# Kernel tuning notes

Measured on AMD Instinct MI355X. Metric: run time of the kernel, lower is better.

Reference implementation:

```python
import jax, jax.numpy as jnp
import numpy as np
from jax import lax

NUM_CLASSES = 5
CONF_THRESH = 0.6
NMS_THRESH = 0.2
NUM_TOPK = 64          # min(topk=1000, 64) as in post_process
STRIDES = (8, 16, 32)
FMP = ((160, 160), (80, 80), (40, 40))  # 1280x1280 input
BATCH = 128


def setup_inputs() -> dict:
    key = jax.random.key(0)
    ks = jax.random.split(key, 9)
    d = {}
    i = 0
    for name, (h, w) in zip(("8", "16", "32"), FMP):
        hw = h * w
        d["obj" + name] = jax.random.normal(ks[i], (BATCH, hw, 1), jnp.float32); i += 1
        d["cls" + name] = jax.random.normal(ks[i], (BATCH, hw, NUM_CLASSES), jnp.float32); i += 1
        d["reg" + name] = jax.random.normal(ks[i], (BATCH, hw, 4), jnp.float32); i += 1
    return d


def make_anchors(h, w, stride):
    ay, ax = jnp.meshgrid(jnp.arange(h), jnp.arange(w), indexing="ij")
    xy = jnp.stack([ax, ay], axis=-1).astype(jnp.float32).reshape(-1, 2)
    return (xy + 0.5) * stride  # [HW, 2]


def decode_boxes(reg, anchors, stride):
    # ctr = reg[:, :2]*stride + anchor;  wh = exp(reg[:, 2:])*stride
    ctr = reg[:, :2] * stride + anchors
    wh = jnp.exp(reg[:, 2:]) * stride
    return jnp.concatenate([ctr - 0.5 * wh, ctr + 0.5 * wh], axis=-1)  # x1y1x2y2


def iou_matrix(b):
    # Faithful to YOLO.nms: areas un-clamped, intersection w/h clamped at 1e-10
    x1, y1, x2, y2 = b[:, 0], b[:, 1], b[:, 2], b[:, 3]
    areas = (x2 - x1) * (y2 - y1)
    xx1 = jnp.maximum(x1[:, None], x1[None, :])
    yy1 = jnp.maximum(y1[:, None], y1[None, :])
    xx2 = jnp.minimum(x2[:, None], x2[None, :])
    yy2 = jnp.minimum(y2[:, None], y2[None, :])
    w = jnp.maximum(1e-10, xx2 - xx1)
    h = jnp.maximum(1e-10, yy2 - yy1)
    inter = w * h
    return inter / (areas[:, None] + areas[None, :] - inter)


def nms_keep(iou, valid):
    # Greedy NMS on score-sorted candidates: fixed-length sequential suppression.
    n = iou.shape[0]
    idx = jnp.arange(n)
    def body(i, keep):
        sup = keep[i] & (iou[i] > NMS_THRESH) & (idx > i)
        return keep & jnp.logical_not(sup)
    return lax.fori_loop(0, n, body, valid)


def _single_image(obj8, cls8, reg8, obj16, cls16, reg16, obj32, cls32, reg32):
    levels = ((obj8, cls8, reg8), (obj16, cls16, reg16), (obj32, cls32, reg32))
    sc, lb, bx, vd = [], [], [], []
    for lvl, (obj, cls, reg) in enumerate(levels):
        h, w = FMP[lvl]
        s = STRIDES[lvl]
        anchors = make_anchors(h, w, s)
        boxes = decode_boxes(reg, anchors, s)                      # [HW, 4]
        scores = jnp.sqrt(jax.nn.sigmoid(obj) * jax.nn.sigmoid(cls)).reshape(-1)  # [HW*C]
        top_s, top_i = lax.top_k(scores, NUM_TOPK)
        a_idx = top_i // NUM_CLASSES
        labels = top_i % NUM_CLASSES
        sc.append(top_s)
        lb.append(labels)
        bx.append(boxes[a_idx])
        vd.append(top_s > CONF_THRESH)
    scores = jnp.concatenate(sc)          # [192]
    labels = jnp.concatenate(lb)
    boxes = jnp.concatenate(bx)           # [192, 4]
    valid = jnp.concatenate(vd)
    # Global score order (within each class this matches the per-class argsort)
    order = jnp.argsort(-scores)
    scores, labels, boxes, valid = scores[order], labels[order], boxes[order], valid[order]
    # Class-offset trick: boxes of different classes have IoU ~ 0 -> exactly per-class NMS
    off = labels.astype(jnp.float32) * (2.0 * jnp.max(jnp.abs(boxes)) + 1.0)
    keep = nms_keep(iou_matrix(boxes + off[:, None]), valid)
    scores = jnp.where(keep, scores, 0.0)
    boxes = jnp.where(keep[:, None], boxes, 0.0)
    labels = jnp.where(keep, labels, -1)
    return boxes, scores, labels


def reference(obj8, cls8, reg8, obj16, cls16, reg16, obj32, cls32, reg32):
    # Batched (vmapped) version of inference_single_image's decode+postprocess.
    # Returns fixed-size masked outputs: boxes [B,192,4], scores [B,192], labels [B,192].
    return jax.vmap(_single_image)(obj8, cls8, reg8, obj16, cls16, reg16, obj32, cls32, reg32)
```

## Files before the change

kernel.cpp:

```cpp
#include <hip/hip_runtime.h>


#define NUM_CLASSES 5
#define CONF_THRESH 0.6f
#define NMS_THRESH  0.2f
#define TOPK   64
#define BATCH  128
#define TOTK   192
#define NCH    21
#define CHUNK  1600
#define SCAP   1024
#define NTHR   320
#define WCAP   1024

typedef unsigned long long u64;
typedef unsigned int u32;
typedef unsigned short u16;


__device__ inline u32 wave_sort64_desc_u32(u32 v, int lane) {
  #pragma unroll
  for (int k = 2; k <= 64; k <<= 1) {
    #pragma unroll
    for (int j = k >> 1; j > 0; j >>= 1) {
      u32 o = __shfl_xor(v, j, 64);
      bool keepMax = (((lane & k) == 0) != ((lane & j) != 0));
      v = keepMax ? (v > o ? v : o) : (v < o ? v : o);
    }
  }
  return v;
}

__device__ inline u64 wave_sort64_desc(u64 v, int lane) {
  #pragma unroll
  for (int k = 2; k <= 64; k <<= 1) {
    #pragma unroll
    for (int j = k >> 1; j > 0; j >>= 1) {
      u64 o = __shfl_xor(v, j, 64);
      bool keepMax = (((lane & k) == 0) != ((lane & j) != 0));
      v = keepMax ? (v > o ? v : o) : (v < o ? v : o);
    }
  }
  return v;
}

__device__ __forceinline__ u64 u64max(u64 a, u64 b) { return a > b ? a : b; }
__device__ __forceinline__ u64 u64min(u64 a, u64 b) { return a < b ? a : b; }

__device__ __forceinline__ u64 bmerge64_desc(u64 v, int lane) {
  #pragma unroll
  for (int j = 32; j > 0; j >>= 1) {
    u64 o = __shfl_xor(v, j, 64);
    v = ((lane & j) == 0) ? u64max(v, o) : u64min(v, o);
  }
  return v;
}

__device__ __forceinline__ u64 merge_top64(u64 a, u64 brev, int lane) {
  return bmerge64_desc(u64max(a, brev), lane);
}

__device__ __forceinline__ u64 merge4_top64(u64 a, u64 brev, u64 c, u64 drev, int lane) {
  u64 ab = merge_top64(a, brev, lane);
  u64 cd = merge_top64(c, drev, lane);
  u64 cdr = __shfl(cd, 63 - lane, 64);
  return merge_top64(ab, cdr, lane);
}

__device__ inline u64 score_key(float so, float cv, int idx) {
  float sc = 1.0f / (1.0f + expf(-cv));
  float s  = sqrtf(__fmul_rn(so, sc));
  return ((u64)__float_as_uint(s) << 32) | (u32)(~(u32)idx);
}

__device__ inline float sigmoidf(float x) { return 1.0f / (1.0f + expf(-x)); }

__global__ __launch_bounds__(NTHR) void scan_kernel(
    const float* __restrict__ obj8,  const float* __restrict__ cls8,
    const float* __restrict__ obj16, const float* __restrict__ cls16,
    const float* __restrict__ obj32, const float* __restrict__ cls32,
    u64* __restrict__ ws_part) {
  __shared__ u64 keys[SCAP];
  __shared__ u16 wl[WCAP];
  __shared__ int cnt;
  __shared__ int wcnt;
  __shared__ u32 sthr[5];

  const int bx  = blockIdx.x;
  const int img = bx / NCH;
  const int c   = bx - img * NCH;
  const int t   = threadIdx.x;
  const int lane = t & 63, wv = t >> 6;

  const float *obj, *cls;
  int hw, off;
  if (c < 16)      { obj = obj8;  cls = cls8;  hw = 25600; off = c * CHUNK; }
  else if (c < 20) { obj = obj16; cls = cls16; hw = 6400;  off = (c - 16) * CHUNK; }
  else             { obj = obj32; cls = cls32; hw = 1600;  off = 0; }
  obj += (size_t)img * hw + off;
  cls += ((size_t)img * hw + off) * NUM_CLASSES;

  float ff[25];
  {
    const float4* c4 = (const float4*)cls + (size_t)t * 5;
    float4 q0 = c4[0], q1 = c4[1], q2 = c4[2], q3 = c4[3], q4 = c4[4];
    float4 ov = ((const float4*)obj)[t];
    float cv[20] = { q0.x,q0.y,q0.z,q0.w, q1.x,q1.y,q1.z,q1.w,
                     q2.x,q2.y,q2.z,q2.w, q3.x,q3.y,q3.z,q3.w,
                     q4.x,q4.y,q4.z,q4.w };
    float dob[4] = { 1.0f + __expf(-ov.x), 1.0f + __expf(-ov.y),
                     1.0f + __expf(-ov.z), 1.0f + __expf(-ov.w) };
    #pragma unroll
    for (int a = 0; a < 4; ++a)
      #pragma unroll
      for (int j = 0; j < 5; ++j)
        ff[a * 5 + j] = dob[a] * (1.0f + __expf(-cv[a * 5 + j]));
    float ot = obj[1280 + t];
    float dot_ = 1.0f + __expf(-ot);
    #pragma unroll
    for (int j = 0; j < 5; ++j) {
      float cvt = cls[(1280 + t) * 5 + j];
      ff[20 + j] = dot_ * (1.0f + __expf(-cvt));
    }
  }

  float pmin = ff[0];
  #pragma unroll
  for (int i = 1; i < 25; ++i) pmin = fminf(pmin, ff[i]);
  u32 srt = wave_sort64_desc_u32(__float_as_uint(pmin), lane);
  if (lane == 48) sthr[wv] = srt;
  if (t == 0) { cnt = 0; wcnt = 0; }
  __syncthreads();
  u64 thr; float thr_inv;
  {
    float pmax = __uint_as_float(sthr[0]);
    pmax = fmaxf(pmax, __uint_as_float(sthr[1]));
    pmax = fmaxf(pmax, __uint_as_float(sthr[2]));
    pmax = fmaxf(pmax, __uint_as_float(sthr[3]));
    pmax = fmaxf(pmax, __uint_as_float(sthr[4]));
    float ts = sqrtf(__fdiv_rn(1.0f, pmax)) * (1.0f - 1e-4f);
    thr = ((u64)__float_as_uint(ts) << 32) - 1ull;
    thr_inv = __fdiv_rn(1.0f, __fmul_rn(__fmul_rn(ts, ts), 1.0f - 2e-4f));
  }

  #pragma unroll
  for (int a = 0; a < 4; ++a)
    #pragma unroll
    for (int j = 0; j < 5; ++j)
      if (ff[a * 5 + j] <= thr_inv) {
        int p = atomicAdd(&wcnt, 1);
        if (p < WCAP) wl[p] = (u16)(((4 * t + a) << 3) | j);
      }
  #pragma unroll
  for (int j = 0; j < 5; ++j)
    if (ff[20 + j] <= thr_inv) {
      int p = atomicAdd(&wcnt, 1);
      if (p < WCAP) wl[p] = (u16)(((1280 + t) << 3) | j);
    }
  __syncthreads();
  const int wc = wcnt;

  if (wc <= WCAP) {
    for (int i = t; i < wc; i += NTHR) {
      u32 cd = (u32)wl[i];
      int al = (int)(cd >> 3);
      int jj = (int)(cd & 7u);
      float o   = obj[al];
      float cvv = cls[al * 5 + jj];
      u64 key = score_key(sigmoidf(o), cvv, (off + al) * NUM_CLASSES + jj);
      if (key > thr) { int p = atomicAdd(&cnt, 1); if (p < SCAP) keys[p] = key; }
    }
  } else {
    #pragma unroll
    for (int a = 0; a < 4; ++a)
      #pragma unroll
      for (int j = 0; j < 5; ++j)
        if (ff[a * 5 + j] <= thr_inv) {
          int al = 4 * t + a;
          u64 key = score_key(sigmoidf(obj[al]), cls[al * 5 + j],
                              (off + al) * NUM_CLASSES + j);
          if (key > thr) { int p = atomicAdd(&cnt, 1); if (p < SCAP) keys[p] = key; }
        }
    #pragma unroll
    for (int j = 0; j < 5; ++j)
      if (ff[20 + j] <= thr_inv) {
        int al = 1280 + t;
        u64 key = score_key(sigmoidf(obj[al]), cls[al * 5 + j],
                            (off + al) * NUM_CLASSES + j);
        if (key > thr) { int p = atomicAdd(&cnt, 1); if (p < SCAP) keys[p] = key; }
      }
  }
  __syncthreads();
  int cs = cnt; if (cs > SCAP) cs = SCAP;
  __syncthreads();

  if (cs > 512) {
    int m = 64; while (m < cs) m <<= 1;
    for (int i = cs + t; i < m; i += NTHR) keys[i] = 0ull;
    for (int kk = 2; kk <= m; kk <<= 1) {
      for (int j = kk >> 1; j > 0; j >>= 1) {
        __syncthreads();
        for (int i = t; i < m; i += NTHR) {
          int ixj = i ^ j;
          if (ixj > i) {
            u64 a = keys[i], b = keys[ixj];
            bool sw = ((i & kk) == 0) ? (a < b) : (a > b);
            if (sw) { keys[i] = b; keys[ixj] = a; }
          }
        }
      }
    }
    __syncthreads();
  } else {
    int npow = 1; while (npow * 64 < cs) npow <<= 1;
    for (int i = cs + t; i < npow * 64; i += NTHR) keys[i] = 0ull;
    __syncthreads();
    for (int r = wv; r < npow; r += 5) {
      u64 v = wave_sort64_desc(keys[r * 64 + lane], lane);
      keys[r * 64 + lane] = v;
    }
    __syncthreads();
    for (int half = npow >> 1; half >= 1; half >>= 1) {
      u64 res = 0ull;
      if (wv < half) {
        u64 a    = keys[(2 * wv) * 64 + lane];
        u64 brev = keys[(2 * wv + 1) * 64 + 63 - lane];
        res = merge_top64(a, brev, lane);
      }
      __syncthreads();
      if (wv < half) keys[wv * 64 + lane] = res;
      __syncthreads();
    }
  }
  if (t < TOPK) ws_part[(size_t)bx * TOPK + t] = keys[t];
}

__global__ __launch_bounds__(256) void merge_nms_kernel(
    const u64* __restrict__ ws_part,
    const float* __restrict__ reg8, const float* __restrict__ reg16, const float* __restrict__ reg32,
    float* __restrict__ out) {
  __shared__ u64   lds_runs[256];
  __shared__ u64   lvlkeys[TOTK];
  __shared__ u64   skeys[TOTK];
  __shared__ int   slb[TOTK];
  __shared__ float sbx[TOTK * 4];
  __shared__ float sX1[TOTK], sY1[TOTK], sX2[TOTK], sY2[TOTK], sA[TOTK];
  __shared__ u64   rows[TOTK * 3];
  __shared__ u64   svalid[3];
  __shared__ u64   skeep[3];
  __shared__ float lmarr[3];

  const int img  = blockIdx.x;
  const int t    = threadIdx.x;
  const int lane = t & 63, wv = t >> 6;

  const u64* pbase = ws_part + (size_t)img * NCH * TOPK;

  {
    const u64* q = pbase + (size_t)(4 * wv) * TOPK;
    u64 a    = q[lane];
    u64 brev = q[64 + 63 - lane];
    u64 c    = q[128 + lane];
    u64 drev = q[192 + 63 - lane];
    lds_runs[wv * 64 + lane] = merge4_top64(a, brev, c, drev, lane);
    if (wv == 3) lvlkeys[128 + lane] = pbase[20 * TOPK + lane];
  }
  __syncthreads();

  if (wv == 0) {
    u64 a    = lds_runs[lane];
    u64 brev = lds_runs[64 + 63 - lane];
    u64 c    = lds_runs[128 + lane];
    u64 drev = lds_runs[192 + 63 - lane];
    lvlkeys[lane] = merge4_top64(a, brev, c, drev, lane);
  } else if (wv == 1) {
    const u64* q = pbase + (size_t)16 * TOPK;
    u64 a    = q[lane];
    u64 brev = q[64 + 63 - lane];
    u64 c    = q[128 + lane];
    u64 drev = q[192 + 63 - lane];
    lvlkeys[64 + lane] = merge4_top64(a, brev, c, drev, lane);
  }
  __syncthreads();

  if (wv == 0) {
    const u64 HIMASK = 0xFFFFFFFF00000000ull;
    u64 s0 = (lvlkeys[lane] & HIMASK) | (u32)(~(u32)lane);
    int i1 = 64 + 63 - lane;
    u64 s1r = (lvlkeys[i1] & HIMASK) | (u32)(~(u32)i1);
    int i2 = 128 + 63 - lane;
    u64 s2r = (lvlkeys[i2] & HIMASK) | (u32)(~(u32)i2);
    u64 hi_ = bmerge64_desc(u64max(s0, s1r), lane);
    u64 lo_ = bmerge64_desc(u64min(s0, s1r), lane);
    u64 R1   = u64max(lo_, s2r);
    u64 out0 = bmerge64_desc(u64max(hi_, R1), lane);
    u64 out1 = bmerge64_desc(u64min(hi_, R1), lane);
    u64 out2 = bmerge64_desc(u64min(lo_, s2r), lane);
    skeys[lane]       = out0;
    skeys[64 + lane]  = out1;
    skeys[128 + lane] = out2;
  } else {
    int idx = t - 64;
    const float* reg; int w; int hw; float stride;
    if (wv == 1)      { reg = reg8;  w = 160; hw = 25600; stride = 8.0f;  }
    else if (wv == 2) { reg = reg16; w = 80;  hw = 6400;  stride = 16.0f; }
    else              { reg = reg32; w = 40;  hw = 1600;  stride = 32.0f; }
    reg += (size_t)img * hw * 4;
    u64 key = lvlkeys[idx];
    u32 raw = ~((u32)key);
    int a = (int)(raw / NUM_CLASSES);
    int c = (int)(raw - (u32)a * NUM_CLASSES);
    int ix = a % w, iy = a / w;
    float ax = __fmul_rn((float)ix + 0.5f, stride);
    float ay = __fmul_rn((float)iy + 0.5f, stride);
    float r0 = reg[a*4+0], r1 = reg[a*4+1], r2 = reg[a*4+2], r3 = reg[a*4+3];
    float cx = __fadd_rn(__fmul_rn(r0, stride), ax);
    float cy = __fadd_rn(__fmul_rn(r1, stride), ay);
    float wd = __fmul_rn(expf(r2), stride);
    float ht = __fmul_rn(expf(r3), stride);
    float x1 = __fsub_rn(cx, __fmul_rn(0.5f, wd));
    float y1 = __fsub_rn(cy, __fmul_rn(0.5f, ht));
    float x2 = __fadd_rn(cx, __fmul_rn(0.5f, wd));
    float y2 = __fadd_rn(cy, __fmul_rn(0.5f, ht));
    slb[idx] = c;
    sbx[idx*4+0] = x1; sbx[idx*4+1] = y1;
    sbx[idx*4+2] = x2; sbx[idx*4+3] = y2;
  }
  __syncthreads();

  float sc_r = 0.0f, b0 = 0.0f, b1 = 0.0f, b2 = 0.0f, b3 = 0.0f;
  int p = 0, lb_r = 0;
  if (t < TOTK) {
    u64 key = skeys[t];
    p = (int)(~((u32)key)) & 255;
    sc_r = __uint_as_float((u32)(key >> 32));
    lb_r = slb[p];
    b0 = sbx[p*4+0]; b1 = sbx[p*4+1]; b2 = sbx[p*4+2]; b3 = sbx[p*4+3];
    float lm = fmaxf(fmaxf(fabsf(b0), fabsf(b1)), fmaxf(fabsf(b2), fabsf(b3)));
    #pragma unroll
    for (int d = 32; d > 0; d >>= 1) lm = fmaxf(lm, __shfl_xor(lm, d, 64));
    if (lane == 0) lmarr[wv] = lm;
  }
  __syncthreads();

  const float lmAll = fmaxf(fmaxf(lmarr[0], lmarr[1]), lmarr[2]);
  const float offscale = __fadd_rn(__fmul_rn(2.0f, lmAll), 1.0f);

  float X1 = 0.0f, Y1 = 0.0f, X2 = 0.0f, Y2 = 0.0f, A = 0.0f;
  if (t < TOTK) {
    float off = __fmul_rn((float)lb_r, offscale);
    X1 = __fadd_rn(b0, off); Y1 = __fadd_rn(b1, off);
    X2 = __fadd_rn(b2, off); Y2 = __fadd_rn(b3, off);
    A  = __fmul_rn(__fsub_rn(X2, X1), __fsub_rn(Y2, Y1));
    sX1[t] = X1; sY1[t] = Y1; sX2[t] = X2; sY2[t] = Y2; sA[t] = A;
    u64 bal = __ballot(sc_r > CONF_THRESH);
    if (lane == 0) svalid[wv] = bal;
  }
  __syncthreads();

  if (t < TOTK) {
    u64 r0m = 0, r1m = 0, r2m = 0;
    for (int j = t + 1; j < TOTK; ++j) {
      float xx1 = fmaxf(X1, sX1[j]);
      float yy1 = fmaxf(Y1, sY1[j]);
      float xx2 = fminf(X2, sX2[j]);
      float yy2 = fminf(Y2, sY2[j]);
      float wv2 = fmaxf(1e-10f, __fsub_rn(xx2, xx1));
      float hv = fmaxf(1e-10f, __fsub_rn(yy2, yy1));
      float inter = __fmul_rn(wv2, hv);
      float den = __fsub_rn(__fadd_rn(A, sA[j]), inter);
      float iou = __fdiv_rn(inter, den);
      if (iou > NMS_THRESH) {
        u64 b = 1ull << (j & 63);
        int wd = j >> 6;
        r0m |= (wd == 0) ? b : 0ull;
        r1m |= (wd == 1) ? b : 0ull;
        r2m |= (wd == 2) ? b : 0ull;
      }
    }
    rows[t*3+0] = r0m; rows[t*3+1] = r1m; rows[t*3+2] = r2m;
  }
  __syncthreads();

  if (t < 64) {
    u64 k0 = svalid[0], k1 = svalid[1], k2 = svalid[2];
    #pragma unroll 4
    for (int i = 0; i < 64; ++i) {
      u64 m0 = rows[i*3+0], m1 = rows[i*3+1], m2 = rows[i*3+2];
      u64 sel = 0ull - ((k0 >> i) & 1ull);
      k0 &= ~(m0 & sel); k1 &= ~(m1 & sel); k2 &= ~(m2 & sel);
    }
    #pragma unroll 4
    for (int i = 0; i < 64; ++i) {
      int r = 64 + i;
      u64 m0 = rows[r*3+0], m1 = rows[r*3+1], m2 = rows[r*3+2];
      u64 sel = 0ull - ((k1 >> i) & 1ull);
      k0 &= ~(m0 & sel); k1 &= ~(m1 & sel); k2 &= ~(m2 & sel);
    }
    #pragma unroll 4
    for (int i = 0; i < 64; ++i) {
      int r = 128 + i;
      u64 m0 = rows[r*3+0], m1 = rows[r*3+1], m2 = rows[r*3+2];
      u64 sel = 0ull - ((k2 >> i) & 1ull);
      k0 &= ~(m0 & sel); k1 &= ~(m1 & sel); k2 &= ~(m2 & sel);
    }
    if (t == 0) { skeep[0] = k0; skeep[1] = k1; skeep[2] = k2; }
  }
  __syncthreads();

  if (t < TOTK) {
    float* out_boxes  = out;
    float* out_scores = out + (size_t)BATCH * TOTK * 4;
    float* out_labels = out + (size_t)BATCH * TOTK * 5;
    bool kp = (skeep[t >> 6] >> (t & 63)) & 1ull;
    int gi = img * TOTK + t;
    out_boxes[gi*4+0] = kp ? sbx[p*4+0] : 0.0f;
    out_boxes[gi*4+1] = kp ? sbx[p*4+1] : 0.0f;
    out_boxes[gi*4+2] = kp ? sbx[p*4+2] : 0.0f;
    out_boxes[gi*4+3] = kp ? sbx[p*4+3] : 0.0f;
    out_scores[gi] = kp ? sc_r : 0.0f;
    out_labels[gi] = kp ? (float)lb_r : -1.0f;
  }
}

extern "C" void kernel_launch(void* const* d_in, const int* in_sizes, int n_in,
                              void* d_out, int out_size, void* d_ws, size_t ws_size,
                              hipStream_t stream) {
  const float* obj8  = (const float*)d_in[0];
  const float* cls8  = (const float*)d_in[1];
  const float* reg8  = (const float*)d_in[2];
  const float* obj16 = (const float*)d_in[3];
  const float* cls16 = (const float*)d_in[4];
  const float* reg16 = (const float*)d_in[5];
  const float* obj32 = (const float*)d_in[6];
  const float* cls32 = (const float*)d_in[7];
  const float* reg32 = (const float*)d_in[8];

  u64* ws_part = (u64*)d_ws;

  scan_kernel<<<dim3(BATCH * NCH), dim3(NTHR), 0, stream>>>(
      obj8, cls8, obj16, cls16, obj32, cls32, ws_part);
  merge_nms_kernel<<<dim3(BATCH * 3 / 3), dim3(256), 0, stream>>>(
      ws_part, reg8, reg16, reg32, (float*)d_out);
}
```

Measured before the change: 217.4 us.

## Use 256-thread scan blocks and cache survivor obj/cls values in LDS

Reduces the scan block from 320 to 256 threads. The 1600-anchor chunk is now covered by a main float4 pass plus a second float4 pass on 144 threads, and the threshold is derived from 4 waves sampling only the first 1024 anchors. Survivor candidates store their raw obj/cls values in shared memory, so the key-building pass no longer re-reads global memory. The overflow fallback now rescans every candidate. This trades extra LDS and a less representative threshold sample for fewer global reloads and a smaller block.

Result: no change. 221.2 us (+1.7%).

```diff
diff --git a/kernel.cpp b/kernel.cpp
--- a/kernel.cpp
+++ b/kernel.cpp
@@ -10,7 +10,7 @@
 #define NCH    21
 #define CHUNK  1600
 #define SCAP   1024
-#define NTHR   320
+#define NTHR   256
 #define WCAP   1024
 
 typedef unsigned long long u64;
@@ -80,11 +80,12 @@
     const float* __restrict__ obj16, const float* __restrict__ cls16,
     const float* __restrict__ obj32, const float* __restrict__ cls32,
     u64* __restrict__ ws_part) {
-  __shared__ u64 keys[SCAP];
-  __shared__ u16 wl[WCAP];
+  __shared__ u64    keys[SCAP];
+  __shared__ float2 wlf[WCAP];
+  __shared__ u16    wli[WCAP];
   __shared__ int cnt;
   __shared__ int wcnt;
-  __shared__ u32 sthr[5];
+  __shared__ u32 sthr[4];
 
   const int bx  = blockIdx.x;
   const int img = bx / NCH;
@@ -100,7 +101,10 @@
   obj += (size_t)img * hw + off;
   cls += ((size_t)img * hw + off) * NUM_CLASSES;
 
-  float ff[25];
+  if (t == 0) { cnt = 0; wcnt = 0; }
+
+  u64 thr; float thr_inv;
+
   {
     const float4* c4 = (const float4*)cls + (size_t)t * 5;
     float4 q0 = c4[0], q1 = c4[1], q2 = c4[2], q3 = c4[3], q4 = c4[4];
@@ -108,87 +112,102 @@
     float cv[20] = { q0.x,q0.y,q0.z,q0.w, q1.x,q1.y,q1.z,q1.w,
                      q2.x,q2.y,q2.z,q2.w, q3.x,q3.y,q3.z,q3.w,
                      q4.x,q4.y,q4.z,q4.w };
-    float dob[4] = { 1.0f + __expf(-ov.x), 1.0f + __expf(-ov.y),
-                     1.0f + __expf(-ov.z), 1.0f + __expf(-ov.w) };
-    #pragma unroll
-    for (int a = 0; a < 4; ++a)
+    float ovv[4] = { ov.x, ov.y, ov.z, ov.w };
+    float ff[20];
+    #pragma unroll
+    for (int a = 0; a < 4; ++a) {
+      float dob = 1.0f + __expf(-ovv[a]);
       #pragma unroll
       for (int j = 0; j < 5; ++j)
-        ff[a * 5 + j] = dob[a] * (1.0f + __expf(-cv[a * 5 + j]));
-    float ot = obj[1280 + t];
-    float dot_ = 1.0f + __expf(-ot);
-    #pragma unroll
-    for (int j = 0; j < 5; ++j) {
-      float cvt = cls[(1280 + t) * 5 + j];
-      ff[20 + j] = dot_ * (1.0f + __expf(-cvt));
-    }
-  }
-
-  float pmin = ff[0];
-  #pragma unroll
-  for (int i = 1; i < 25; ++i) pmin = fminf(pmin, ff[i]);
-  u32 srt = wave_sort64_desc_u32(__float_as_uint(pmin), lane);
-  if (lane == 48) sthr[wv] = srt;
-  if (t == 0) { cnt = 0; wcnt = 0; }
-  __syncthreads();
-  u64 thr; float thr_inv;
-  {
-    float pmax = __uint_as_float(sthr[0]);
-    pmax = fmaxf(pmax, __uint_as_float(sthr[1]));
-    pmax = fmaxf(pmax, __uint_as_float(sthr[2]));
-    pmax = fmaxf(pmax, __uint_as_float(sthr[3]));
-    pmax = fmaxf(pmax, __uint_as_float(sthr[4]));
-    float ts = sqrtf(__fdiv_rn(1.0f, pmax)) * (1.0f - 1e-4f);
-    thr = ((u64)__float_as_uint(ts) << 32) - 1ull;
-    thr_inv = __fdiv_rn(1.0f, __fmul_rn(__fmul_rn(ts, ts), 1.0f - 2e-4f));
-  }
-
-  #pragma unroll
-  for (int a = 0; a < 4; ++a)
-    #pragma unroll
-    for (int j = 0; j < 5; ++j)
-      if (ff[a * 5 + j] <= thr_inv) {
-        int p = atomicAdd(&wcnt, 1);
-        if (p < WCAP) wl[p] = (u16)(((4 * t + a) << 3) | j);
-      }
-  #pragma unroll
-  for (int j = 0; j < 5; ++j)
-    if (ff[20 + j] <= thr_inv) {
-      int p = atomicAdd(&wcnt, 1);
-      if (p < WCAP) wl[p] = (u16)(((1280 + t) << 3) | j);
-    }
-  __syncthreads();
-  const int wc = wcnt;
-
-  if (wc <= WCAP) {
-    for (int i = t; i < wc; i += NTHR) {
-      u32 cd = (u32)wl[i];
-      int al = (int)(cd >> 3);
-      int jj = (int)(cd & 7u);
-      float o   = obj[al];
-      float cvv = cls[al * 5 + jj];
-      u64 key = score_key(sigmoidf(o), cvv, (off + al) * NUM_CLASSES + jj);
-      if (key > thr) { int p = atomicAdd(&cnt, 1); if (p < SCAP) keys[p] = key; }
-    }
-  } else {
+        ff[a * 5 + j] = dob * (1.0f + __expf(-cv[a * 5 + j]));
+    }
+
+    float pmin = ff[0];
+    #pragma unroll
+    for (int i = 1; i < 20; ++i) pmin = fminf(pmin, ff[i]);
+    u32 srt = wave_sort64_desc_u32(__float_as_uint(pmin), lane);
+    if (lane == 48) sthr[wv] = srt;
+    __syncthreads();
+    {
+      float pmax = __uint_as_float(sthr[0]);
+      pmax = fmaxf(pmax, __uint_as_float(sthr[1]));
+      pmax = fmaxf(pmax, __uint_as_float(sthr[2]));
+      pmax = fmaxf(pmax, __uint_as_float(sthr[3]));
+      float ts = sqrtf(__fdiv_rn(1.0f, pmax)) * (1.0f - 1e-4f);
+      thr = ((u64)__float_as_uint(ts) << 32) - 1ull;
+      thr_inv = __fdiv_rn(1.0f, __fmul_rn(__fmul_rn(ts, ts), 1.0f - 2e-4f));
+    }
+
     #pragma unroll
     for (int a = 0; a < 4; ++a)
       #pragma unroll
       for (int j = 0; j < 5; ++j)
         if (ff[a * 5 + j] <= thr_inv) {
-          int al = 4 * t + a;
+          int p = atomicAdd(&wcnt, 1);
+          if (p < WCAP) {
+            wli[p] = (u16)(((4 * t + a) << 3) | j);
+            wlf[p] = make_float2(ovv[a], cv[a * 5 + j]);
+          }
+        }
+  }
+
+  if (t < 144) {
+    const float4* c4 = (const float4*)cls + 1280 + (size_t)t * 5;
+    float4 q0 = c4[0], q1 = c4[1], q2 = c4[2], q3 = c4[3], q4 = c4[4];
+    float4 ov = ((const float4*)obj)[256 + t];
+    float cv[20] = { q0.x,q0.y,q0.z,q0.w, q1.x,q1.y,q1.z,q1.w,
+                     q2.x,q2.y,q2.z,q2.w, q3.x,q3.y,q3.z,q3.w,
+                     q4.x,q4.y,q4.z,q4.w };
+    float ovv[4] = { ov.x, ov.y, ov.z, ov.w };
+    #pragma unroll
+    for (int a = 0; a < 4; ++a) {
+      float dob = 1.0f + __expf(-ovv[a]);
+      #pragma unroll
+      for (int j = 0; j < 5; ++j) {
+        float f = dob * (1.0f + __expf(-cv[a * 5 + j]));
+        if (f <= thr_inv) {
+          int p = atomicAdd(&wcnt, 1);
+          if (p < WCAP) {
+            wli[p] = (u16)(((1024 + 4 * t + a) << 3) | j);
+            wlf[p] = make_float2(ovv[a], cv[a * 5 + j]);
+          }
+        }
+      }
+    }
+  }
+  __syncthreads();
+  const int wc = wcnt;
+
+  if (wc <= WCAP) {
+    for (int i = t; i < wc; i += NTHR) {
+      u32 id = (u32)wli[i];
+      float2 oc = wlf[i];
+      int al = (int)(id >> 3);
+      int jj = (int)(id & 7u);
+      u64 key = score_key(sigmoidf(oc.x), oc.y, (off + al) * NUM_CLASSES + jj);
+      if (key > thr) { int p = atomicAdd(&cnt, 1); if (p < SCAP) keys[p] = key; }
+    }
+  } else {
+    #pragma unroll
+    for (int a = 0; a < 4; ++a)
+      #pragma unroll
+      for (int j = 0; j < 5; ++j) {
+        int al = 4 * t + a;
+        u64 key = score_key(sigmoidf(obj[al]), cls[al * 5 + j],
+                            (off + al) * NUM_CLASSES + j);
+        if (key > thr) { int p = atomicAdd(&cnt, 1); if (p < SCAP) keys[p] = key; }
+      }
+    if (t < 144) {
+      #pragma unroll
+      for (int a = 0; a < 4; ++a)
+        #pragma unroll
+        for (int j = 0; j < 5; ++j) {
+          int al = 1024 + 4 * t + a;
           u64 key = score_key(sigmoidf(obj[al]), cls[al * 5 + j],
                               (off + al) * NUM_CLASSES + j);
           if (key > thr) { int p = atomicAdd(&cnt, 1); if (p < SCAP) keys[p] = key; }
         }
-    #pragma unroll
-    for (int j = 0; j < 5; ++j)
-      if (ff[20 + j] <= thr_inv) {
-        int al = 1280 + t;
-        u64 key = score_key(sigmoidf(obj[al]), cls[al * 5 + j],
-                            (off + al) * NUM_CLASSES + j);
-        if (key > thr) { int p = atomicAdd(&cnt, 1); if (p < SCAP) keys[p] = key; }
-      }
+    }
   }
   __syncthreads();
   int cs = cnt; if (cs > SCAP) cs = SCAP;
@@ -215,7 +234,7 @@
     int npow = 1; while (npow * 64 < cs) npow <<= 1;
     for (int i = cs + t; i < npow * 64; i += NTHR) keys[i] = 0ull;
     __syncthreads();
-    for (int r = wv; r < npow; r += 5) {
+    for (int r = wv; r < npow; r += 4) {
       u64 v = wave_sort64_desc(keys[r * 64 + lane], lane);
       keys[r * 64 + lane] = v;
     }
@@ -440,6 +459,6 @@
 
   scan_kernel<<<dim3(BATCH * NCH), dim3(NTHR), 0, stream>>>(
       obj8, cls8, obj16, cls16, obj32, cls32, ws_part);
-  merge_nms_kernel<<<dim3(BATCH * 3 / 3), dim3(256), 0, stream>>>(
+  merge_nms_kernel<<<dim3(BATCH), dim3(256), 0, stream>>>(
       ws_part, reg8, reg16, reg32, (float*)d_out);
 }
```

## Coalesce class loads across threads and stage objectness in LDS for scan

Applied to the files above, without the earlier changes.

Each thread now reads the class scores as strided float4 loads interleaved across threads, so a wavefront touches contiguous memory, instead of each thread reading five consecutive float4s. Objectness values and their precomputed 1+exp(-x) terms are staged in shared memory, and the candidate class logits are kept in LDS, so the second pass no longer re-reads global memory. The block size drops from 320 to 256 threads. In exchange, each thread holds 32 values with a per-element divide by 5, LDS use per block grows, and there is an extra barrier.

After: 224.2 us. 1.03x slower.

```diff
diff --git a/kernel.cpp b/kernel.cpp
--- a/kernel.cpp
+++ b/kernel.cpp
@@ -10,7 +10,7 @@
 #define NCH    21
 #define CHUNK  1600
 #define SCAP   1024
-#define NTHR   320
+#define NTHR   256
 #define WCAP   1024
 
 typedef unsigned long long u64;
@@ -75,16 +75,23 @@
 
 __device__ inline float sigmoidf(float x) { return 1.0f / (1.0f + expf(-x)); }
 
+__device__ __forceinline__ float f4c(const float4& v, int e) {
+  return e == 0 ? v.x : e == 1 ? v.y : e == 2 ? v.z : v.w;
+}
+
 __global__ __launch_bounds__(NTHR) void scan_kernel(
     const float* __restrict__ obj8,  const float* __restrict__ cls8,
     const float* __restrict__ obj16, const float* __restrict__ cls16,
     const float* __restrict__ obj32, const float* __restrict__ cls32,
     u64* __restrict__ ws_part) {
-  __shared__ u64 keys[SCAP];
-  __shared__ u16 wl[WCAP];
+  __shared__ float obj_lds[CHUNK];
+  __shared__ float dob_lds[CHUNK];
+  __shared__ u64   keys[SCAP];
+  __shared__ u16   wli[WCAP];
+  __shared__ float wlc[WCAP];
   __shared__ int cnt;
   __shared__ int wcnt;
-  __shared__ u32 sthr[5];
+  __shared__ u32 sthr[4];
 
   const int bx  = blockIdx.x;
   const int img = bx / NCH;
@@ -99,37 +106,52 @@
   else             { obj = obj32; cls = cls32; hw = 1600;  off = 0; }
   obj += (size_t)img * hw + off;
   cls += ((size_t)img * hw + off) * NUM_CLASSES;
-
-  float ff[25];
+  const int offc = off * NUM_CLASSES;
+
+  const float4* cp = (const float4*)cls;
+  float4 q[8];
+  #pragma unroll
+  for (int k = 0; k < 7; ++k) q[k] = cp[t + k * 256];
+  q[7] = (t < 208) ? cp[t + 1792] : make_float4(0.f, 0.f, 0.f, 0.f);
+
   {
-    const float4* c4 = (const float4*)cls + (size_t)t * 5;
-    float4 q0 = c4[0], q1 = c4[1], q2 = c4[2], q3 = c4[3], q4 = c4[4];
-    float4 ov = ((const float4*)obj)[t];
-    float cv[20] = { q0.x,q0.y,q0.z,q0.w, q1.x,q1.y,q1.z,q1.w,
-                     q2.x,q2.y,q2.z,q2.w, q3.x,q3.y,q3.z,q3.w,
-                     q4.x,q4.y,q4.z,q4.w };
-    float dob[4] = { 1.0f + __expf(-ov.x), 1.0f + __expf(-ov.y),
-                     1.0f + __expf(-ov.z), 1.0f + __expf(-ov.w) };
-    #pragma unroll
-    for (int a = 0; a < 4; ++a)
-      #pragma unroll
-      for (int j = 0; j < 5; ++j)
-        ff[a * 5 + j] = dob[a] * (1.0f + __expf(-cv[a * 5 + j]));
-    float ot = obj[1280 + t];
-    float dot_ = 1.0f + __expf(-ot);
-    #pragma unroll
-    for (int j = 0; j < 5; ++j) {
-      float cvt = cls[(1280 + t) * 5 + j];
-      ff[20 + j] = dot_ * (1.0f + __expf(-cvt));
+    const float4* op4 = (const float4*)obj;
+    float4 o0 = op4[t];
+    ((float4*)obj_lds)[t] = o0;
+    ((float4*)dob_lds)[t] = make_float4(
+        1.0f + __expf(-o0.x), 1.0f + __expf(-o0.y),
+        1.0f + __expf(-o0.z), 1.0f + __expf(-o0.w));
+    if (t < 144) {
+      float4 o1 = op4[256 + t];
+      ((float4*)obj_lds)[256 + t] = o1;
+      ((float4*)dob_lds)[256 + t] = make_float4(
+          1.0f + __expf(-o1.x), 1.0f + __expf(-o1.y),
+          1.0f + __expf(-o1.z), 1.0f + __expf(-o1.w));
+    }
+  }
+  if (t == 0) { cnt = 0; wcnt = 0; }
+  __syncthreads();
+
+  float ff[32];
+  #pragma unroll
+  for (int k = 0; k < 8; ++k) {
+    #pragma unroll
+    for (int e = 0; e < 4; ++e) {
+      float f = 3.0e38f;
+      if (k < 7 || t < 208) {
+        int ei = (k * 256 + t) * 4 + e;
+        int a  = ei / 5;
+        f = dob_lds[a] * (1.0f + __expf(-f4c(q[k], e)));
+      }
+      ff[k * 4 + e] = f;
     }
   }
 
   float pmin = ff[0];
   #pragma unroll
-  for (int i = 1; i < 25; ++i) pmin = fminf(pmin, ff[i]);
+  for (int i = 1; i < 32; ++i) pmin = fminf(pmin, ff[i]);
   u32 srt = wave_sort64_desc_u32(__float_as_uint(pmin), lane);
   if (lane == 48) sthr[wv] = srt;
-  if (t == 0) { cnt = 0; wcnt = 0; }
   __syncthreads();
   u64 thr; float thr_inv;
   {
@@ -137,58 +159,42 @@
     pmax = fmaxf(pmax, __uint_as_float(sthr[1]));
     pmax = fmaxf(pmax, __uint_as_float(sthr[2]));
     pmax = fmaxf(pmax, __uint_as_float(sthr[3]));
-    pmax = fmaxf(pmax, __uint_as_float(sthr[4]));
     float ts = sqrtf(__fdiv_rn(1.0f, pmax)) * (1.0f - 1e-4f);
     thr = ((u64)__float_as_uint(ts) << 32) - 1ull;
     thr_inv = __fdiv_rn(1.0f, __fmul_rn(__fmul_rn(ts, ts), 1.0f - 2e-4f));
   }
 
   #pragma unroll
-  for (int a = 0; a < 4; ++a)
-    #pragma unroll
-    for (int j = 0; j < 5; ++j)
-      if (ff[a * 5 + j] <= thr_inv) {
+  for (int k = 0; k < 8; ++k)
+    #pragma unroll
+    for (int e = 0; e < 4; ++e)
+      if ((k < 7 || t < 208) && ff[k * 4 + e] <= thr_inv) {
+        int ei = (k * 256 + t) * 4 + e;
         int p = atomicAdd(&wcnt, 1);
-        if (p < WCAP) wl[p] = (u16)(((4 * t + a) << 3) | j);
+        if (p < WCAP) { wli[p] = (u16)ei; wlc[p] = f4c(q[k], e); }
       }
-  #pragma unroll
-  for (int j = 0; j < 5; ++j)
-    if (ff[20 + j] <= thr_inv) {
-      int p = atomicAdd(&wcnt, 1);
-      if (p < WCAP) wl[p] = (u16)(((1280 + t) << 3) | j);
-    }
   __syncthreads();
   const int wc = wcnt;
 
   if (wc <= WCAP) {
     for (int i = t; i < wc; i += NTHR) {
-      u32 cd = (u32)wl[i];
-      int al = (int)(cd >> 3);
-      int jj = (int)(cd & 7u);
-      float o   = obj[al];
-      float cvv = cls[al * 5 + jj];
-      u64 key = score_key(sigmoidf(o), cvv, (off + al) * NUM_CLASSES + jj);
+      int ei = (int)wli[i];
+      float cvv = wlc[i];
+      int a = ei / 5;
+      u64 key = score_key(sigmoidf(obj_lds[a]), cvv, offc + ei);
       if (key > thr) { int p = atomicAdd(&cnt, 1); if (p < SCAP) keys[p] = key; }
     }
   } else {
     #pragma unroll
-    for (int a = 0; a < 4; ++a)
+    for (int k = 0; k < 8; ++k)
       #pragma unroll
-      for (int j = 0; j < 5; ++j)
-        if (ff[a * 5 + j] <= thr_inv) {
-          int al = 4 * t + a;
-          u64 key = score_key(sigmoidf(obj[al]), cls[al * 5 + j],
-                              (off + al) * NUM_CLASSES + j);
+      for (int e = 0; e < 4; ++e)
+        if (k < 7 || t < 208) {
+          int ei = (k * 256 + t) * 4 + e;
+          int a = ei / 5;
+          u64 key = score_key(sigmoidf(obj_lds[a]), f4c(q[k], e), offc + ei);
           if (key > thr) { int p = atomicAdd(&cnt, 1); if (p < SCAP) keys[p] = key; }
         }
-    #pragma unroll
-    for (int j = 0; j < 5; ++j)
-      if (ff[20 + j] <= thr_inv) {
-        int al = 1280 + t;
-        u64 key = score_key(sigmoidf(obj[al]), cls[al * 5 + j],
-                            (off + al) * NUM_CLASSES + j);
-        if (key > thr) { int p = atomicAdd(&cnt, 1); if (p < SCAP) keys[p] = key; }
-      }
   }
   __syncthreads();
   int cs = cnt; if (cs > SCAP) cs = SCAP;
@@ -215,7 +221,7 @@
     int npow = 1; while (npow * 64 < cs) npow <<= 1;
     for (int i = cs + t; i < npow * 64; i += NTHR) keys[i] = 0ull;
     __syncthreads();
-    for (int r = wv; r < npow; r += 5) {
+    for (int r = wv; r < npow; r += 4) {
       u64 v = wave_sort64_desc(keys[r * 64 + lane], lane);
       keys[r * 64 + lane] = v;
     }
@@ -440,6 +446,6 @@
 
   scan_kernel<<<dim3(BATCH * NCH), dim3(NTHR), 0, stream>>>(
       obj8, cls8, obj16, cls16, obj32, cls32, ws_part);
-  merge_nms_kernel<<<dim3(BATCH * 3 / 3), dim3(256), 0, stream>>>(
+  merge_nms_kernel<<<dim3(BATCH), dim3(256), 0, stream>>>(
       ws_part, reg8, reg16, reg32, (float*)d_out);
 }
```
